# Performance work log

Measured on AMD Instinct MI355X. Metric: run time of the kernel, lower is better.

The kernel has to match this reference:

```python
import jax, jax.numpy as jnp
import numpy as np

B, S, D, H = 4, 2048, 768, 12
HD = D // H  # head_dim = 64


def setup_inputs() -> dict:
    key = jax.random.key(0)
    ks = jax.random.split(key, 5)
    scale = 0.02
    return {
        "x": jax.random.normal(ks[0], (B, S, D), dtype=jnp.float32),
        "wq": jax.random.normal(ks[1], (D, D), dtype=jnp.float32) * scale,
        "wk": jax.random.normal(ks[2], (D, D), dtype=jnp.float32) * scale,
        "wv": jax.random.normal(ks[3], (D, D), dtype=jnp.float32) * scale,
        "wo": jax.random.normal(ks[4], (D, D), dtype=jnp.float32) * scale,
        "bo": jnp.zeros((D,), dtype=jnp.float32),
    }


def reference(x, wq, wk, wv, wo, bo):
    b, s, d = x.shape
    # torch Linear: y = x @ W.T ; qkv_bias=False
    q = (x @ wq.T).reshape(b, s, H, HD).transpose(0, 2, 1, 3)  # [b,h,s,hd]
    k = (x @ wk.T).reshape(b, s, H, HD).transpose(0, 2, 1, 3)
    v = (x @ wv.T).reshape(b, s, H, HD).transpose(0, 2, 1, 3)
    scores = jnp.einsum("bhqd,bhkd->bhqk", q, k)  # full [b,h,s,s] score matrix
    causal = jnp.triu(jnp.ones((s, s), dtype=bool), k=1)
    scores = jnp.where(causal, -jnp.inf, scores)
    attn = jax.nn.softmax(scores / jnp.sqrt(jnp.float32(HD)), axis=-1)
    ctx = jnp.einsum("bhqk,bhkd->bhqd", attn, v)
    ctx = ctx.transpose(0, 2, 1, 3).reshape(b, s, d)
    return ctx @ wo.T + bo  # dropout is identity in eval mode
```

## Files before the change

### kernel.cpp

```cpp
#include <hip/hip_runtime.h>

#define H 12
#define S 2048
#define D 768
#define HD 64
#define BATCH 4
#define M_TOT (BATCH * S)

typedef __attribute__((ext_vector_type(8))) short bf16x8;
typedef __attribute__((ext_vector_type(4))) float f32x4;

__device__ __forceinline__ ushort f2bf(float f) {
  unsigned int x = __float_as_uint(f);
  x += 0x7fffu + ((x >> 16) & 1u);
  return (ushort)(x >> 16);
}

__device__ __forceinline__ uint cvt_pk_bf16(float lo, float hi) {
  uint r;
  asm("v_cvt_pk_bf16_f32 %0, %1, %2" : "=v"(r) : "v"(lo), "v"(hi));
  return r;
}

__device__ __forceinline__ void gload_lds16(const void* gsrc, void* lds) {
  __builtin_amdgcn_global_load_lds(
      (const __attribute__((address_space(1))) unsigned int*)gsrc,
      (__attribute__((address_space(3))) unsigned int*)lds, 16, 0, 0);
}

__global__ __launch_bounds__(256) void cast_all(
    const float* __restrict__ x, const float* __restrict__ wq,
    const float* __restrict__ wk, const float* __restrict__ wv,
    const float* __restrict__ wo, ushort* __restrict__ xb,
    ushort* __restrict__ wqb, ushort* __restrict__ wkb,
    ushort* __restrict__ wvb, ushort* __restrict__ wob) {
  const int NX = M_TOT * D / 4;
  const int NW = D * D / 4;
  int i = blockIdx.x * 256 + threadIdx.x;
  const float* src; ushort* dst; int off;
  if (i < NX) { src = x; dst = xb; off = i; }
  else {
    int j = i - NX; int w = j / NW; off = j - w * NW;
    src = (w == 0) ? wq : (w == 1) ? wk : (w == 2) ? wv : wo;
    dst = (w == 0) ? wqb : (w == 1) ? wkb : (w == 2) ? wvb : wob;
  }
  float4 f = reinterpret_cast<const float4*>(src)[off];
  ushort4 u;
  u.x = f2bf(f.x); u.y = f2bf(f.y); u.z = f2bf(f.z); u.w = f2bf(f.w);
  reinterpret_cast<ushort4*>(dst)[off] = u;
}

__global__ __launch_bounds__(256, 3) void gemm_qkv(
    const ushort* __restrict__ xb, const ushort* __restrict__ wqb,
    const ushort* __restrict__ wkb, const ushort* __restrict__ wvb,
    ushort* __restrict__ qb, ushort* __restrict__ kb_,
    ushort* __restrict__ vtb, float qscale) {
  __shared__ ushort SM[2][10240];
  const int tid = threadIdx.x;
  const int lane = tid & 63, wid = tid >> 6;
  const int g = lane >> 4, li = lane & 15;

  const int wg = blockIdx.x;
  const int mt = wg & 63, slab = wg >> 6;
  const int m0 = mt * 128, n0 = slab * 64;

  const ushort* xm = xb + (size_t)m0 * 768;
  const ushort* wqn = wqb + (size_t)n0 * 768;
  const ushort* wkn = wkb + (size_t)n0 * 768;
  const ushort* wvn = wvb + (size_t)n0 * 768;

  const int rsub = lane >> 2;
  const int coff = (((lane & 3) ^ ((rsub >> 1) & 3)) << 3);
  const int wrow = wid * 16;

  auto stage = [&](int buf, int k0) {
#pragma unroll
    for (int rnd = 0; rnd < 2; ++rnd) {
      const int row0 = rnd * 64 + wrow;
      gload_lds16(&xm[(size_t)(row0 + rsub) * 768 + k0 + coff], &SM[buf][row0 * 32]);
    }
    gload_lds16(&wqn[(size_t)(wrow + rsub) * 768 + k0 + coff], &SM[buf][4096 + wrow * 32]);
    gload_lds16(&wkn[(size_t)(wrow + rsub) * 768 + k0 + coff], &SM[buf][6144 + wrow * 32]);
    gload_lds16(&wvn[(size_t)(wrow + rsub) * 768 + k0 + coff], &SM[buf][8192 + wrow * 32]);
  };

  f32x4 acc[3][2][4] = {};
  stage(0, 0);

  for (int kt = 0; kt < 24; ++kt) {
    const int cur = kt & 1;
    asm volatile("s_waitcnt vmcnt(0)" ::: "memory");
    __syncthreads();
    if (kt + 1 < 24) stage(cur ^ 1, (kt + 1) * 32);

    const ushort* bp = &SM[cur][0];
    bf16x8 a[2];
#pragma unroll
    for (int i = 0; i < 2; ++i) {
      const int row = wid * 32 + i * 16 + li;
      a[i] = *reinterpret_cast<const bf16x8*>(
          &bp[row * 32 + ((g ^ ((row >> 1) & 3)) << 3)]);
    }
#pragma unroll
    for (int o = 0; o < 3; ++o) {
      const int off = 4096 + o * 2048;
      bf16x8 b[4];
#pragma unroll
      for (int j = 0; j < 4; ++j) {
        const int row = j * 16 + li;
        b[j] = *reinterpret_cast<const bf16x8*>(
            &bp[off + row * 32 + ((g ^ ((row >> 1) & 3)) << 3)]);
      }
      __builtin_amdgcn_s_setprio(1);
#pragma unroll
      for (int i = 0; i < 2; ++i)
#pragma unroll
        for (int j = 0; j < 4; ++j)
          acc[o][i][j] = __builtin_amdgcn_mfma_f32_16x16x32_bf16(a[i], b[j], acc[o][i][j], 0, 0, 0);
      __builtin_amdgcn_s_setprio(0);
    }
  }

  ushort* Cs = &SM[0][0];
  const int b0 = m0 >> 11, sb = m0 & 2047;

  __syncthreads();
#pragma unroll
  for (int o = 0; o < 2; ++o)
#pragma unroll
    for (int i = 0; i < 2; ++i)
#pragma unroll
      for (int j = 0; j < 4; ++j)
#pragma unroll
        for (int rr = 0; rr < 4; ++rr) {
          const int row = wid * 32 + i * 16 + g * 4 + rr;
          const int col = j * 16 + li;
          const int pc = ((((col >> 3) ^ (row & 7)) << 3) | (col & 7));
          const float v = acc[o][i][j][rr] * (o == 0 ? qscale : 1.0f);
          Cs[o * 8192 + row * 64 + pc] = f2bf(v);
        }
  __syncthreads();
  {
    const int row = tid >> 1, half = tid & 1;
    const int m = m0 + row;
    const size_t rb = (((size_t)b0 * H + slab) * S + (m & 2047)) * HD + half * 32;
    ushort* dq = &qb[rb];
    ushort* dk = &kb_[rb];
#pragma unroll
    for (int c8 = 0; c8 < 4; ++c8) {
      const int col = half * 32 + c8 * 8;
      const int chunk = (col >> 3) ^ (row & 7);
      *reinterpret_cast<bf16x8*>(&dq[c8 * 8]) =
          *reinterpret_cast<const bf16x8*>(&Cs[row * 64 + chunk * 8]);
      *reinterpret_cast<bf16x8*>(&dk[c8 * 8]) =
          *reinterpret_cast<const bf16x8*>(&Cs[8192 + row * 64 + chunk * 8]);
    }
  }

  __syncthreads();
#pragma unroll
  for (int i = 0; i < 2; ++i)
#pragma unroll
    for (int j = 0; j < 4; ++j)
#pragma unroll
      for (int rr = 0; rr < 4; ++rr) {
        const int tok = wid * 32 + i * 16 + g * 4 + rr;
        const int feat = j * 16 + li;
        const int pc = ((((tok >> 3) ^ (feat & 7)) << 3) | (tok & 7));
        Cs[feat * 128 + pc] = f2bf(acc[2][i][j][rr]);
      }
  __syncthreads();
  {
    const int feat = tid >> 2, qtr = tid & 3;
    ushort* dv = &vtb[(((size_t)b0 * H + slab) * HD + feat) * S + sb + qtr * 32];
#pragma unroll
    for (int c8 = 0; c8 < 4; ++c8) {
      const int tok = qtr * 32 + c8 * 8;
      const int chunk = (tok >> 3) ^ (feat & 7);
      *reinterpret_cast<bf16x8*>(&dv[c8 * 8]) =
          *reinterpret_cast<const bf16x8*>(&Cs[feat * 128 + chunk * 8]);
    }
  }
}

__global__ __launch_bounds__(256) void gemm_wo(const ushort* __restrict__ A,
                                               const ushort* __restrict__ W,
                                               float* __restrict__ out_f,
                                               const float* __restrict__ bias) {
  __shared__ ushort SM[3][6144];
  const int tid = threadIdx.x;
  const int lane = tid & 63, wid = tid >> 6;
  const int g = lane >> 4, li = lane & 15;
  const int wm = wid >> 1, wn = wid & 1;
  const int m0 = blockIdx.x * 64, n0 = blockIdx.y * 128;

  const int rsub = lane >> 2;
  const int coff = (((lane & 3) ^ ((rsub >> 1) & 3)) << 3);

  auto stage = [&](int buf, int k0) {
    gload_lds16(&A[(size_t)(m0 + wid * 16 + rsub) * 768 + k0 + coff],
                &SM[buf][wid * 16 * 32]);
#pragma unroll
    for (int rnd = 0; rnd < 2; ++rnd) {
      const int row0 = rnd * 64 + wid * 16;
      gload_lds16(&W[(size_t)(n0 + row0 + rsub) * 768 + k0 + coff],
                  &SM[buf][2048 + row0 * 32]);
    }
  };

  f32x4 acc[2][4] = {};
  stage(0, 0);
  stage(1, 32);

  int cur = 0, pre = 2;
  for (int kt = 0; kt < 24; ++kt) {
    if (kt < 23) asm volatile("s_waitcnt vmcnt(3) lgkmcnt(0)" ::: "memory");
    else         asm volatile("s_waitcnt vmcnt(0) lgkmcnt(0)" ::: "memory");
    __builtin_amdgcn_s_barrier();
    if (kt + 2 < 24) stage(pre, (kt + 2) * 32);

    bf16x8 a[2], b[4];
#pragma unroll
    for (int i = 0; i < 2; ++i) {
      const int row = wm * 32 + i * 16 + li;
      a[i] = *reinterpret_cast<const bf16x8*>(
          &SM[cur][row * 32 + ((g ^ ((row >> 1) & 3)) << 3)]);
    }
#pragma unroll
    for (int j = 0; j < 4; ++j) {
      const int row = wn * 64 + j * 16 + li;
      b[j] = *reinterpret_cast<const bf16x8*>(
          &SM[cur][2048 + row * 32 + ((g ^ ((row >> 1) & 3)) << 3)]);
    }
    __builtin_amdgcn_s_setprio(1);
#pragma unroll
    for (int i = 0; i < 2; ++i)
#pragma unroll
      for (int j = 0; j < 4; ++j)
        acc[i][j] = __builtin_amdgcn_mfma_f32_16x16x32_bf16(a[i], b[j], acc[i][j], 0, 0, 0);
    __builtin_amdgcn_s_setprio(0);

    cur = (cur == 2) ? 0 : cur + 1;
    pre = (pre == 2) ? 0 : pre + 1;
  }

#pragma unroll
  for (int i = 0; i < 2; ++i)
#pragma unroll
    for (int j = 0; j < 4; ++j)
#pragma unroll
      for (int r = 0; r < 4; ++r) {
        const int m = m0 + wm * 32 + i * 16 + g * 4 + r;
        const int n = n0 + wn * 64 + j * 16 + li;
        out_f[(size_t)m * 768 + n] = acc[i][j][r] + bias[n];
      }
}

__global__ __launch_bounds__(256) void attn_kernel(const ushort* __restrict__ Q,
                                                   const ushort* __restrict__ K,
                                                   const ushort* __restrict__ VT,
                                                   ushort* __restrict__ ctx) {
  __shared__ ushort Ks[2][64 * 64];
  __shared__ ushort Vts[2][64 * 64];
  __shared__ ushort Ps[4][32][72];

  const int tid = threadIdx.x;
  const int lane = tid & 63, wid = tid >> 6;
  const int g = lane >> 4, li = lane & 15;

  const int wg = blockIdx.x;
  const int xcd = wg & 7, t = wg >> 3;
  const int bh = xcd + 8 * (t >> 4);
  const int p = t & 15;
  const int qL = 64 * (31 - p), qS = 64 * p;

  const size_t base = (size_t)bh * S * HD;
  const size_t vtbase = (size_t)bh * HD * S;

  bf16x8 aq[2][2];
#pragma unroll
  for (int f = 0; f < 2; ++f) {
    const size_t qr = base + (size_t)((f ? qS : qL) + wid * 16 + li) * HD;
#pragma unroll
    for (int c = 0; c < 2; ++c)
      aq[f][c] = *reinterpret_cast<const bf16x8*>(&Q[qr + c * 32 + g * 8]);
  }

  f32x4 acc[2][4] = {};
  float lpart[2] = {0.f, 0.f};

  const int nkt = 32 - p;

  const int rsub = lane >> 3;
  const int c8e = (((lane & 7) ^ rsub) << 3);

  auto stage = [&](int buf, int k0) {
#pragma unroll
    for (int rnd = 0; rnd < 2; ++rnd) {
      const int row0 = rnd * 32 + wid * 8;
      gload_lds16(&K[base + (size_t)(k0 + row0 + rsub) * HD + c8e], &Ks[buf][row0 << 6]);
      gload_lds16(&VT[vtbase + (size_t)(row0 + rsub) * S + k0 + c8e], &Vts[buf][row0 << 6]);
    }
  };

  stage(0, 0);

  for (int kt = 0; kt < nkt; ++kt) {
    const int cur = kt & 1;
    const int k0 = kt * 64;
    const bool doS = (kt <= p);

    asm volatile("s_waitcnt vmcnt(0)" ::: "memory");
    __syncthreads();
    if (kt + 1 < nkt) stage(cur ^ 1, k0 + 64);

    f32x4 sc[2][4];
    __builtin_amdgcn_s_setprio(1);
#pragma unroll
    for (int ct = 0; ct < 4; ++ct) {
      const int row = ct * 16 + li, r7 = row & 7;
      const ushort* kr = &Ks[cur][row << 6];
      bf16x8 kb0 = *reinterpret_cast<const bf16x8*>(&kr[(g ^ r7) << 3]);
      bf16x8 kb1 = *reinterpret_cast<const bf16x8*>(&kr[((4 + g) ^ r7) << 3]);
      {
        f32x4 z = {};
        z = __builtin_amdgcn_mfma_f32_16x16x32_bf16(kb0, aq[0][0], z, 0, 0, 0);
        z = __builtin_amdgcn_mfma_f32_16x16x32_bf16(kb1, aq[0][1], z, 0, 0, 0);
        sc[0][ct] = z;
      }
      if (doS) {
        f32x4 z = {};
        z = __builtin_amdgcn_mfma_f32_16x16x32_bf16(kb0, aq[1][0], z, 0, 0, 0);
        z = __builtin_amdgcn_mfma_f32_16x16x32_bf16(kb1, aq[1][1], z, 0, 0, 0);
        sc[1][ct] = z;
      }
    }
    __builtin_amdgcn_s_setprio(0);

    if (kt == nkt - 1) {
      const int q = qL + wid * 16 + li;
#pragma unroll
      for (int ct = 0; ct < 4; ++ct)
#pragma unroll
        for (int r = 0; r < 4; ++r)
          if (k0 + ct * 16 + 4 * g + r > q) sc[0][ct][r] = -1e30f;
    }
    if (kt == p) {
      const int q = qS + wid * 16 + li;
#pragma unroll
      for (int ct = 0; ct < 4; ++ct)
#pragma unroll
        for (int r = 0; r < 4; ++r)
          if (k0 + ct * 16 + 4 * g + r > q) sc[1][ct][r] = -1e30f;
    }

#pragma unroll
    for (int f = 0; f < 2; ++f) {
      if (f == 1 && !doS) break;
#pragma unroll
      for (int ct = 0; ct < 4; ++ct) {
        float p0 = __builtin_amdgcn_exp2f(sc[f][ct][0]);
        float p1 = __builtin_amdgcn_exp2f(sc[f][ct][1]);
        float p2 = __builtin_amdgcn_exp2f(sc[f][ct][2]);
        float p3 = __builtin_amdgcn_exp2f(sc[f][ct][3]);
        lpart[f] += (p0 + p1) + (p2 + p3);
        uint2 pw;
        pw.x = cvt_pk_bf16(p0, p1);
        pw.y = cvt_pk_bf16(p2, p3);
        *reinterpret_cast<uint2*>(&Ps[wid][f * 16 + li][ct * 16 + 4 * g]) = pw;
      }
    }

    bf16x8 pa[2][2];
    pa[0][0] = *reinterpret_cast<const bf16x8*>(&Ps[wid][li][g * 8]);
    pa[0][1] = *reinterpret_cast<const bf16x8*>(&Ps[wid][li][32 + g * 8]);
    if (doS) {
      pa[1][0] = *reinterpret_cast<const bf16x8*>(&Ps[wid][16 + li][g * 8]);
      pa[1][1] = *reinterpret_cast<const bf16x8*>(&Ps[wid][16 + li][32 + g * 8]);
    }
    __builtin_amdgcn_s_setprio(1);
#pragma unroll
    for (int dt = 0; dt < 4; ++dt) {
      const int row = dt * 16 + li, r7 = row & 7;
      const ushort* vr = &Vts[cur][row << 6];
      bf16x8 vb0 = *reinterpret_cast<const bf16x8*>(&vr[(g ^ r7) << 3]);
      bf16x8 vb1 = *reinterpret_cast<const bf16x8*>(&vr[((4 + g) ^ r7) << 3]);
      acc[0][dt] = __builtin_amdgcn_mfma_f32_16x16x32_bf16(pa[0][0], vb0, acc[0][dt], 0, 0, 0);
      acc[0][dt] = __builtin_amdgcn_mfma_f32_16x16x32_bf16(pa[0][1], vb1, acc[0][dt], 0, 0, 0);
      if (doS) {
        acc[1][dt] = __builtin_amdgcn_mfma_f32_16x16x32_bf16(pa[1][0], vb0, acc[1][dt], 0, 0, 0);
        acc[1][dt] = __builtin_amdgcn_mfma_f32_16x16x32_bf16(pa[1][1], vb1, acc[1][dt], 0, 0, 0);
      }
    }
    __builtin_amdgcn_s_setprio(0);
  }

  const int b = bh / H, h = bh % H;
#pragma unroll
  for (int f = 0; f < 2; ++f) {
    float l = lpart[f];
    l += __shfl_xor(l, 16);
    l += __shfl_xor(l, 32);
#pragma unroll
    for (int r = 0; r < 4; ++r) {
      float inv = 1.0f / __shfl(l, 4 * g + r);
      const int s = (f ? qS : qL) + wid * 16 + 4 * g + r;
#pragma unroll
      for (int dt = 0; dt < 4; ++dt)
        ctx[((size_t)(b * S + s)) * D + h * HD + dt * 16 + li] =
            f2bf(acc[f][dt][r] * inv);
    }
  }
}

extern "C" void kernel_launch(void* const* d_in, const int* in_sizes, int n_in,
                              void* d_out, int out_size, void* d_ws, size_t ws_size,
                              hipStream_t stream) {
  (void)in_sizes; (void)n_in; (void)out_size; (void)ws_size;
  const float* x  = (const float*)d_in[0];
  const float* wq = (const float*)d_in[1];
  const float* wk = (const float*)d_in[2];
  const float* wv = (const float*)d_in[3];
  const float* wo = (const float*)d_in[4];
  const float* bo = (const float*)d_in[5];
  float* out = (float*)d_out;

  const size_t xn = (size_t)M_TOT * D;
  const size_t wn = (size_t)D * D;

  ushort* p = (ushort*)d_ws;
  ushort* x_bf  = p; p += xn;
  ushort* wq_bf = p; p += wn;
  ushort* wk_bf = p; p += wn;
  ushort* wv_bf = p; p += wn;
  ushort* wo_bf = p; p += wn;
  ushort* q_bf  = p; p += xn;
  ushort* k_bf  = p; p += xn;
  ushort* vt_bf = p; p += xn;
  ushort* ctx_bf = x_bf;

  cast_all<<<8448, 256, 0, stream>>>(x, wq, wk, wv, wo,
                                     x_bf, wq_bf, wk_bf, wv_bf, wo_bf);

  const float QSCALE = 0.125f * 1.44269504f;
  gemm_qkv<<<768, 256, 0, stream>>>(x_bf, wq_bf, wk_bf, wv_bf,
                                    q_bf, k_bf, vt_bf, QSCALE);

  attn_kernel<<<768, 256, 0, stream>>>(q_bf, k_bf, vt_bf, ctx_bf);

  gemm_wo<<<dim3(128, 6), 256, 0, stream>>>(ctx_bf, wo_bf, out, bo);
}
```

Baseline: 126.5 us.

## Split long causal attention query tiles across two workgroups with a combine pass

Replaces the paired long/short query-tile scheme with one query tile per workgroup. The 16 longest tiles per head are split into two key-range halves, each writing unnormalized bf16 partial outputs and row sums into the output buffer as scratch, and a new combine kernel merges them. The grid grows from 768 to 2304 workgroups to improve load balance and occupancy. The cost is an extra kernel launch, extra global traffic for the partials, and a bf16 rounding of partial sums before combining.

```diff
diff --git a/kernel.cpp b/kernel.cpp
--- a/kernel.cpp
+++ b/kernel.cpp
@@ -14,6 +14,10 @@
   unsigned int x = __float_as_uint(f);
   x += 0x7fffu + ((x >> 16) & 1u);
   return (ushort)(x >> 16);
+}
+
+__device__ __forceinline__ float bf2f(ushort u) {
+  return __uint_as_float(((unsigned int)u) << 16);
 }
 
 __device__ __forceinline__ uint cvt_pk_bf16(float lo, float hi) {
@@ -259,37 +263,53 @@
 __global__ __launch_bounds__(256) void attn_kernel(const ushort* __restrict__ Q,
                                                    const ushort* __restrict__ K,
                                                    const ushort* __restrict__ VT,
-                                                   ushort* __restrict__ ctx) {
+                                                   ushort* __restrict__ ctx,
+                                                   ushort* __restrict__ po,
+                                                   float* __restrict__ lbuf) {
   __shared__ ushort Ks[2][64 * 64];
   __shared__ ushort Vts[2][64 * 64];
-  __shared__ ushort Ps[4][32][72];
+  __shared__ ushort Ps[4][16][72];
 
   const int tid = threadIdx.x;
   const int lane = tid & 63, wid = tid >> 6;
   const int g = lane >> 4, li = lane & 15;
 
   const int wg = blockIdx.x;
-  const int xcd = wg & 7, t = wg >> 3;
-  const int bh = xcd + 8 * (t >> 4);
-  const int p = t & 15;
-  const int qL = 64 * (31 - p), qS = 64 * p;
+  const int xcd = wg & 7;
+  const int rest = wg >> 3;
+  const int headi = rest % 6;
+  const int bh = headi * 8 + xcd;
+  const int js = rest / 6;
+
+  int t, klo, khi;
+  bool split; int half = 0;
+  if (js < 32) {
+    split = true;
+    t = 31 - (js >> 1);
+    half = js & 1;
+    const int h2 = (t + 2) >> 1;
+    klo = half ? h2 : 0;
+    khi = half ? (t + 1) : h2;
+  } else {
+    split = false;
+    t = 47 - js;
+    klo = 0; khi = t + 1;
+  }
+  const int nkt = khi - klo;
+  const int qtile = t * 64;
 
   const size_t base = (size_t)bh * S * HD;
   const size_t vtbase = (size_t)bh * HD * S;
 
-  bf16x8 aq[2][2];
-#pragma unroll
-  for (int f = 0; f < 2; ++f) {
-    const size_t qr = base + (size_t)((f ? qS : qL) + wid * 16 + li) * HD;
-#pragma unroll
-    for (int c = 0; c < 2; ++c)
-      aq[f][c] = *reinterpret_cast<const bf16x8*>(&Q[qr + c * 32 + g * 8]);
-  }
-
-  f32x4 acc[2][4] = {};
-  float lpart[2] = {0.f, 0.f};
-
-  const int nkt = 32 - p;
+  bf16x8 aq0, aq1;
+  {
+    const size_t qr = base + (size_t)(qtile + wid * 16 + li) * HD;
+    aq0 = *reinterpret_cast<const bf16x8*>(&Q[qr + g * 8]);
+    aq1 = *reinterpret_cast<const bf16x8*>(&Q[qr + 32 + g * 8]);
+  }
+
+  f32x4 acc[4] = {};
+  float lpart = 0.f;
 
   const int rsub = lane >> 3;
   const int c8e = (((lane & 7) ^ rsub) << 3);
@@ -303,18 +323,17 @@
     }
   };
 
-  stage(0, 0);
-
-  for (int kt = 0; kt < nkt; ++kt) {
-    const int cur = kt & 1;
-    const int k0 = kt * 64;
-    const bool doS = (kt <= p);
+  stage(0, klo * 64);
+
+  for (int kti = 0; kti < nkt; ++kti) {
+    const int cur = kti & 1;
+    const int k0 = (klo + kti) * 64;
 
     asm volatile("s_waitcnt vmcnt(0)" ::: "memory");
     __syncthreads();
-    if (kt + 1 < nkt) stage(cur ^ 1, k0 + 64);
-
-    f32x4 sc[2][4];
+    if (kti + 1 < nkt) stage(cur ^ 1, k0 + 64);
+
+    f32x4 sc[4];
     __builtin_amdgcn_s_setprio(1);
 #pragma unroll
     for (int ct = 0; ct < 4; ++ct) {
@@ -322,62 +341,37 @@
       const ushort* kr = &Ks[cur][row << 6];
       bf16x8 kb0 = *reinterpret_cast<const bf16x8*>(&kr[(g ^ r7) << 3]);
       bf16x8 kb1 = *reinterpret_cast<const bf16x8*>(&kr[((4 + g) ^ r7) << 3]);
-      {
-        f32x4 z = {};
-        z = __builtin_amdgcn_mfma_f32_16x16x32_bf16(kb0, aq[0][0], z, 0, 0, 0);
-        z = __builtin_amdgcn_mfma_f32_16x16x32_bf16(kb1, aq[0][1], z, 0, 0, 0);
-        sc[0][ct] = z;
-      }
-      if (doS) {
-        f32x4 z = {};
-        z = __builtin_amdgcn_mfma_f32_16x16x32_bf16(kb0, aq[1][0], z, 0, 0, 0);
-        z = __builtin_amdgcn_mfma_f32_16x16x32_bf16(kb1, aq[1][1], z, 0, 0, 0);
-        sc[1][ct] = z;
-      }
+      f32x4 z = {};
+      z = __builtin_amdgcn_mfma_f32_16x16x32_bf16(kb0, aq0, z, 0, 0, 0);
+      z = __builtin_amdgcn_mfma_f32_16x16x32_bf16(kb1, aq1, z, 0, 0, 0);
+      sc[ct] = z;
     }
     __builtin_amdgcn_s_setprio(0);
 
-    if (kt == nkt - 1) {
-      const int q = qL + wid * 16 + li;
+    if (klo + kti == t) {
+      const int q = qtile + wid * 16 + li;
 #pragma unroll
       for (int ct = 0; ct < 4; ++ct)
 #pragma unroll
         for (int r = 0; r < 4; ++r)
-          if (k0 + ct * 16 + 4 * g + r > q) sc[0][ct][r] = -1e30f;
-    }
-    if (kt == p) {
-      const int q = qS + wid * 16 + li;
-#pragma unroll
-      for (int ct = 0; ct < 4; ++ct)
-#pragma unroll
-        for (int r = 0; r < 4; ++r)
-          if (k0 + ct * 16 + 4 * g + r > q) sc[1][ct][r] = -1e30f;
-    }
-
-#pragma unroll
-    for (int f = 0; f < 2; ++f) {
-      if (f == 1 && !doS) break;
-#pragma unroll
-      for (int ct = 0; ct < 4; ++ct) {
-        float p0 = __builtin_amdgcn_exp2f(sc[f][ct][0]);
-        float p1 = __builtin_amdgcn_exp2f(sc[f][ct][1]);
-        float p2 = __builtin_amdgcn_exp2f(sc[f][ct][2]);
-        float p3 = __builtin_amdgcn_exp2f(sc[f][ct][3]);
-        lpart[f] += (p0 + p1) + (p2 + p3);
-        uint2 pw;
-        pw.x = cvt_pk_bf16(p0, p1);
-        pw.y = cvt_pk_bf16(p2, p3);
-        *reinterpret_cast<uint2*>(&Ps[wid][f * 16 + li][ct * 16 + 4 * g]) = pw;
-      }
-    }
-
-    bf16x8 pa[2][2];
-    pa[0][0] = *reinterpret_cast<const bf16x8*>(&Ps[wid][li][g * 8]);
-    pa[0][1] = *reinterpret_cast<const bf16x8*>(&Ps[wid][li][32 + g * 8]);
-    if (doS) {
-      pa[1][0] = *reinterpret_cast<const bf16x8*>(&Ps[wid][16 + li][g * 8]);
-      pa[1][1] = *reinterpret_cast<const bf16x8*>(&Ps[wid][16 + li][32 + g * 8]);
-    }
+          if (k0 + ct * 16 + 4 * g + r > q) sc[ct][r] = -1e30f;
+    }
+
+#pragma unroll
+    for (int ct = 0; ct < 4; ++ct) {
+      float p0 = __builtin_amdgcn_exp2f(sc[ct][0]);
+      float p1 = __builtin_amdgcn_exp2f(sc[ct][1]);
+      float p2 = __builtin_amdgcn_exp2f(sc[ct][2]);
+      float p3 = __builtin_amdgcn_exp2f(sc[ct][3]);
+      lpart += (p0 + p1) + (p2 + p3);
+      uint2 pw;
+      pw.x = cvt_pk_bf16(p0, p1);
+      pw.y = cvt_pk_bf16(p2, p3);
+      *reinterpret_cast<uint2*>(&Ps[wid][li][ct * 16 + 4 * g]) = pw;
+    }
+
+    bf16x8 pa0 = *reinterpret_cast<const bf16x8*>(&Ps[wid][li][g * 8]);
+    bf16x8 pa1 = *reinterpret_cast<const bf16x8*>(&Ps[wid][li][32 + g * 8]);
     __builtin_amdgcn_s_setprio(1);
 #pragma unroll
     for (int dt = 0; dt < 4; ++dt) {
@@ -385,32 +379,69 @@
       const ushort* vr = &Vts[cur][row << 6];
       bf16x8 vb0 = *reinterpret_cast<const bf16x8*>(&vr[(g ^ r7) << 3]);
       bf16x8 vb1 = *reinterpret_cast<const bf16x8*>(&vr[((4 + g) ^ r7) << 3]);
-      acc[0][dt] = __builtin_amdgcn_mfma_f32_16x16x32_bf16(pa[0][0], vb0, acc[0][dt], 0, 0, 0);
-      acc[0][dt] = __builtin_amdgcn_mfma_f32_16x16x32_bf16(pa[0][1], vb1, acc[0][dt], 0, 0, 0);
-      if (doS) {
-        acc[1][dt] = __builtin_amdgcn_mfma_f32_16x16x32_bf16(pa[1][0], vb0, acc[1][dt], 0, 0, 0);
-        acc[1][dt] = __builtin_amdgcn_mfma_f32_16x16x32_bf16(pa[1][1], vb1, acc[1][dt], 0, 0, 0);
-      }
+      acc[dt] = __builtin_amdgcn_mfma_f32_16x16x32_bf16(pa0, vb0, acc[dt], 0, 0, 0);
+      acc[dt] = __builtin_amdgcn_mfma_f32_16x16x32_bf16(pa1, vb1, acc[dt], 0, 0, 0);
     }
     __builtin_amdgcn_s_setprio(0);
   }
 
-  const int b = bh / H, h = bh % H;
-#pragma unroll
-  for (int f = 0; f < 2; ++f) {
-    float l = lpart[f];
-    l += __shfl_xor(l, 16);
-    l += __shfl_xor(l, 32);
+  float l = lpart;
+  l += __shfl_xor(l, 16);
+  l += __shfl_xor(l, 32);
+
+  if (!split) {
+    const int b = bh / H, h = bh % H;
 #pragma unroll
     for (int r = 0; r < 4; ++r) {
       float inv = 1.0f / __shfl(l, 4 * g + r);
-      const int s = (f ? qS : qL) + wid * 16 + 4 * g + r;
+      const int s = qtile + wid * 16 + 4 * g + r;
 #pragma unroll
       for (int dt = 0; dt < 4; ++dt)
         ctx[((size_t)(b * S + s)) * D + h * HD + dt * 16 + li] =
-            f2bf(acc[f][dt][r] * inv);
-    }
-  }
+            f2bf(acc[dt][r] * inv);
+    }
+  } else {
+    const int tileg = bh * 16 + (t - 16);
+    if (lane < 16)
+      lbuf[((size_t)half * 768 + tileg) * 64 + wid * 16 + li] = l;
+    ushort* pb = &po[((size_t)half * 768 + tileg) << 12];
+#pragma unroll
+    for (int r = 0; r < 4; ++r) {
+      const int row = wid * 16 + 4 * g + r;
+#pragma unroll
+      for (int dt = 0; dt < 4; ++dt)
+        pb[row * 64 + dt * 16 + li] = f2bf(acc[dt][r]);
+    }
+  }
+}
+
+__global__ __launch_bounds__(256) void combine_kernel(const ushort* __restrict__ po,
+                                                      const float* __restrict__ lbuf,
+                                                      ushort* __restrict__ ctx) {
+  const int tileg = blockIdx.x;
+  const int bh = tileg >> 4, t = 16 + (tileg & 15);
+  const int b = bh / H, h = bh % H;
+  const int row = threadIdx.x >> 2, q4 = threadIdx.x & 3;
+
+  const float inv = 1.0f / (lbuf[(size_t)tileg * 64 + row] +
+                            lbuf[((size_t)768 + tileg) * 64 + row]);
+  const ushort* p0 = &po[((size_t)tileg << 12) + row * 64 + q4 * 16];
+  const ushort* p1 = &po[(((size_t)768 + tileg) << 12) + row * 64 + q4 * 16];
+  const int s = t * 64 + row;
+  ushort* dst = &ctx[((size_t)(b * S + s)) * D + h * HD + q4 * 16];
+
+  bf16x8 a0 = *reinterpret_cast<const bf16x8*>(p0);
+  bf16x8 a1 = *reinterpret_cast<const bf16x8*>(p0 + 8);
+  bf16x8 b0 = *reinterpret_cast<const bf16x8*>(p1);
+  bf16x8 b1 = *reinterpret_cast<const bf16x8*>(p1 + 8);
+  ushort out[16];
+#pragma unroll
+  for (int e = 0; e < 8; ++e) {
+    out[e]     = f2bf((bf2f((ushort)a0[e]) + bf2f((ushort)b0[e])) * inv);
+    out[8 + e] = f2bf((bf2f((ushort)a1[e]) + bf2f((ushort)b1[e])) * inv);
+  }
+  *reinterpret_cast<bf16x8*>(dst)     = *reinterpret_cast<const bf16x8*>(&out[0]);
+  *reinterpret_cast<bf16x8*>(dst + 8) = *reinterpret_cast<const bf16x8*>(&out[8]);
 }
 
 extern "C" void kernel_launch(void* const* d_in, const int* in_sizes, int n_in,
@@ -439,6 +470,9 @@
   ushort* vt_bf = p; p += xn;
   ushort* ctx_bf = x_bf;
 
+  ushort* po  = (ushort*)d_out;
+  float* lbuf = (float*)(po + 2 * 768 * 4096);
+
   cast_all<<<8448, 256, 0, stream>>>(x, wq, wk, wv, wo,
                                      x_bf, wq_bf, wk_bf, wv_bf, wo_bf);
 
@@ -446,7 +480,8 @@
   gemm_qkv<<<768, 256, 0, stream>>>(x_bf, wq_bf, wk_bf, wv_bf,
                                     q_bf, k_bf, vt_bf, QSCALE);
 
-  attn_kernel<<<768, 256, 0, stream>>>(q_bf, k_bf, vt_bf, ctx_bf);
+  attn_kernel<<<2304, 256, 0, stream>>>(q_bf, k_bf, vt_bf, ctx_bf, po, lbuf);
+  combine_kernel<<<768, 256, 0, stream>>>(po, lbuf, ctx_bf);
 
   gemm_wo<<<dim3(128, 6), 256, 0, stream>>>(ctx_bf, wo_bf, out, bo);
 }
```

After: 131.2 us. 3.7% more time.
